# Performance work log

Measured on AMD Instinct MI355X. Metric: run time of the kernel, lower is better.

Reference implementation:

```python
import jax, jax.numpy as jnp
import numpy as np

NEG_INF = -1e30


def setup_inputs() -> dict:
    key = jax.random.key(0)
    k1, k2, k3, k4 = jax.random.split(key, 4)
    B, T, C, H = 4, 4096, 1024, 64
    x = jax.random.normal(k1, (B, T, C), dtype=jnp.float32)
    Wk = jax.random.normal(k2, (C, H), dtype=jnp.float32) * (C ** -0.5)
    Wq = jax.random.normal(k3, (C, H), dtype=jnp.float32) * (C ** -0.5)
    Wv = jax.random.normal(k4, (C, H), dtype=jnp.float32) * (C ** -0.5)
    return {"x": x, "Wk": Wk, "Wq": Wq, "Wv": Wv}


def reference(x, Wk, Wq, Wv):
    # x: [B, T, C]; Wq/Wk/Wv: [C, H]
    B, T, C = x.shape
    q = jnp.einsum('btc,ch->bth', x, Wq)  # [B,T,H]
    k = jnp.einsum('btc,ch->bth', x, Wk)  # [B,T,H]
    v = jnp.einsum('btc,ch->bth', x, Wv)  # [B,T,H]
    # NOTE: original scales by C**-0.5 (n_embd), not head_size**-0.5.
    scale = jnp.asarray(C, x.dtype) ** -0.5
    wei = jnp.einsum('bth,bsh->bts', q, k) * scale  # [B,T,T]
    causal = jnp.tril(jnp.ones((T, T), dtype=bool))
    wei = jnp.where(causal, wei, NEG_INF)
    wei = jax.nn.softmax(wei, axis=-1)
    # dropout p=0.0 -> identity
    out = jnp.einsum('bts,bsh->bth', wei, v)  # [B,T,H]
    return out
```

## Files before the change

kernel.cpp:

```cpp
#include <hip/hip_runtime.h>
#include <math.h>

typedef short bfx8 __attribute__((ext_vector_type(8)));
typedef short bfx4 __attribute__((ext_vector_type(4)));
typedef float fx4  __attribute__((ext_vector_type(4)));

__device__ __forceinline__ unsigned short f2bf(float f) {
    unsigned int u = __builtin_bit_cast(unsigned int, f);
    u += 0x7FFFu + ((u >> 16) & 1u);
    return (unsigned short)(u >> 16);
}
__device__ __forceinline__ float bf2f(unsigned short s) {
    unsigned int u = ((unsigned int)s) << 16;
    return __builtin_bit_cast(float, u);
}

__global__ __launch_bounds__(256) void wt_prep(const float* __restrict__ Wq,
                                               const float* __restrict__ Wk,
                                               const float* __restrict__ Wv,
                                               unsigned short* __restrict__ wt)
{
    const int k0  = blockIdx.x * 64;
    const int mat = blockIdx.y;
    const float* W = (mat == 0) ? Wq : ((mat == 1) ? Wk : Wv);
    const float scale = (mat == 0) ? (0.03125f * 1.4426950408889634f) : 1.0f;
    __shared__ unsigned short Ls[64 * 68];
    const int t = threadIdx.x;
    #pragma unroll
    for (int i = 0; i < 4; ++i) {
        int idx4 = t + 256 * i;
        int r = idx4 >> 4, c4 = idx4 & 15;
        float4 v = *(const float4*)&W[(size_t)(k0 + r) * 64 + c4 * 4];
        Ls[r * 68 + c4 * 4 + 0] = f2bf(v.x * scale);
        Ls[r * 68 + c4 * 4 + 1] = f2bf(v.y * scale);
        Ls[r * 68 + c4 * 4 + 2] = f2bf(v.z * scale);
        Ls[r * 68 + c4 * 4 + 3] = f2bf(v.w * scale);
    }
    __syncthreads();
    #pragma unroll
    for (int i = 0; i < 2; ++i) {
        int u = t + 256 * i;
        int n = u >> 3, kc = u & 7;
        bfx8 o;
        #pragma unroll
        for (int j = 0; j < 8; ++j) o[j] = (short)Ls[(kc * 8 + j) * 68 + n];
        *(bfx8*)&wt[(size_t)(mat * 64 + n) * 1024 + k0 + kc * 8] = o;
    }
}

__global__ __launch_bounds__(256) void qkv_mfma(
    const float* __restrict__ x, const unsigned short* __restrict__ wt,
    unsigned short* __restrict__ qb, unsigned short* __restrict__ kb,
    unsigned short* __restrict__ vt)
{
    __shared__ alignas(16) char smem[57344];
    const int t = threadIdx.x;
    const int w = t >> 6, l = t & 63, g = l >> 4, li = l & 15;
    const int m0 = blockIdx.x * 32;
    const int rh  = (w & 1) * 16;
    const int nb0 = (w >> 1) * 6;

    fx4 acc[6];
    #pragma unroll
    for (int i = 0; i < 6; ++i) acc[i] = (fx4){0.f, 0.f, 0.f, 0.f};

    float4 xr[2]; bfx8 wr[6];

#define QKV_LOAD(K0) do { \
    _Pragma("unroll") for (int i_ = 0; i_ < 2; ++i_) { int idx4 = t + 256 * i_; int r_ = idx4 >> 4, c4 = idx4 & 15; \
        xr[i_] = *(const float4*)&x[(size_t)(m0 + r_) * 1024 + (K0) + c4 * 4]; } \
    _Pragma("unroll") for (int i_ = 0; i_ < 6; ++i_) { int idx = t + 256 * i_; int n_ = idx >> 3, c_ = idx & 7; \
        wr[i_] = *(const bfx8*)&wt[(size_t)n_ * 1024 + (K0) + c_ * 8]; } \
} while (0)

#define QKV_STORE(BI) do { \
    char* xb_ = smem + (BI) * 4096; \
    char* wb_ = smem + 8192 + (BI) * 24576; \
    _Pragma("unroll") for (int i_ = 0; i_ < 2; ++i_) { int idx4 = t + 256 * i_; int r_ = idx4 >> 4, c4 = idx4 & 15; \
        bfx4 o_; o_[0] = (short)f2bf(xr[i_].x); o_[1] = (short)f2bf(xr[i_].y); \
        o_[2] = (short)f2bf(xr[i_].z); o_[3] = (short)f2bf(xr[i_].w); \
        *(bfx4*)(xb_ + ((r_ * 128 + c4 * 8) ^ ((r_ & 7) << 4))) = o_; } \
    _Pragma("unroll") for (int i_ = 0; i_ < 6; ++i_) { int idx = t + 256 * i_; int n_ = idx >> 3, c_ = idx & 7; \
        *(bfx8*)(wb_ + ((n_ * 128 + c_ * 16) ^ ((n_ & 7) << 4))) = wr[i_]; } \
} while (0)

    QKV_LOAD(0); QKV_STORE(0);
    __syncthreads();

    for (int ch = 0; ch < 16; ++ch) {
        if (ch + 1 < 16) QKV_LOAD((ch + 1) * 64);
        if (ch) __syncthreads();
        char* xb = smem + (ch & 1) * 4096;
        char* wb = smem + 8192 + (ch & 1) * 24576;
        const int arow = rh + li;
        #pragma unroll
        for (int kk = 0; kk < 2; ++kk) {
            bfx8 af = *(bfx8*)(xb + ((arow * 128 + kk * 64 + g * 16) ^ ((arow & 7) << 4)));
            #pragma unroll
            for (int nb = 0; nb < 6; ++nb) {
                int nrow = (nb0 + nb) * 16 + li;
                bfx8 bf = *(bfx8*)(wb + ((nrow * 128 + kk * 64 + g * 16) ^ ((nrow & 7) << 4)));
                acc[nb] = __builtin_amdgcn_mfma_f32_16x16x32_bf16(af, bf, acc[nb], 0, 0, 0);
            }
        }
        if (ch + 1 < 16) QKV_STORE((ch + 1) & 1);
    }

    const int mrow = m0 + rh + g * 4;
    #pragma unroll
    for (int nb = 0; nb < 6; ++nb) {
        const int nbg = nb0 + nb;
        if (nbg < 4) {
            #pragma unroll
            for (int r = 0; r < 4; ++r)
                qb[(size_t)(mrow + r) * 64 + nbg * 16 + li] = f2bf(acc[nb][r]);
        } else if (nbg < 8) {
            #pragma unroll
            for (int r = 0; r < 4; ++r)
                kb[(size_t)(mrow + r) * 64 + (nbg - 4) * 16 + li] = f2bf(acc[nb][r]);
        }
    }

    __syncthreads();
    unsigned short* Vt = (unsigned short*)smem;
    #pragma unroll
    for (int nb = 0; nb < 6; ++nb) {
        const int nbg = nb0 + nb;
        if (nbg >= 8) {
            #pragma unroll
            for (int r = 0; r < 4; ++r)
                Vt[((nbg - 8) * 16 + li) * 40 + g * 8 + (rh >> 2) + r] = f2bf(acc[nb][r]);
        }
    }
    __syncthreads();
    const int bb = m0 >> 12, mt = m0 & 4095;
    {
        int d = t >> 2, c = t & 3;
        *(bfx8*)&vt[((size_t)(bb * 64 + d)) * 4096 + mt + c * 8] = *(bfx8*)&Vt[d * 40 + c * 8];
    }
}

__global__ __launch_bounds__(256, 4) void attn_mfma(
    const unsigned short* __restrict__ qb, const unsigned short* __restrict__ kb,
    const unsigned short* __restrict__ vt,
    unsigned short* __restrict__ pO, float* __restrict__ pml)
{
    __shared__ alignas(16) char smem[34816];
    const int t = threadIdx.x;
    const int w = t >> 6, l = t & 63, g = l >> 4, li = l & 15;
    const int bx = blockIdx.x;

    const int b = bx & 3;
    const int j = bx >> 2;
    int qt, seg, nch;
    if (j < 224) {
        int a = 1;
        #pragma unroll
        for (int aa = 2; aa <= 7; ++aa) if (j >= 4 * aa * (aa - 1)) a = aa;
        const int local = j - 4 * a * (a - 1);
        qt = 8 * a + local / a;
        seg = local % a;
        nch = 8;
    } else {
        const int jd = j - 224;
        const int r = 7 - (jd >> 3);
        const int a = jd & 7;
        qt = 8 * a + r; seg = a; nch = r + 1;
    }
    const int qbase = qt * 64;
    const int kvb = seg * 512;
    const int qsub = w & 1, par = w >> 1;
    const int qmax_w = qbase + qsub * 32 + 31;
    const int aq = qt >> 3, rq = qt & 7;
    const int slot = b * 288 + (aq + 1) * (4 * aq + rq) + seg;

    const unsigned short* Qg = qb + (size_t)b * 4096 * 64;
    const unsigned short* Kg = kb + (size_t)b * 4096 * 64;
    const unsigned short* Vg = vt + (size_t)b * 64 * 4096;

    bfx8 krg[2], vrg[2];

#define ATT_LOAD(CB) do { \
    _Pragma("unroll") for (int i_ = 0; i_ < 2; ++i_) { int idx = t + 256 * i_; int r_ = idx >> 3, c_ = idx & 7; \
        krg[i_] = *(const bfx8*)&Kg[(size_t)((CB) + r_) * 64 + c_ * 8]; } \
    _Pragma("unroll") for (int i_ = 0; i_ < 2; ++i_) { int idx = t + 256 * i_; int d_ = idx >> 3, c_ = idx & 7; \
        vrg[i_] = *(const bfx8*)&Vg[(size_t)d_ * 4096 + (CB) + c_ * 8]; } \
} while (0)

#define ATT_STORE(BI) do { \
    char* kb_ = smem + (BI) * 8192; \
    char* vb_ = smem + 16384 + (BI) * 8192; \
    _Pragma("unroll") for (int i_ = 0; i_ < 2; ++i_) { int idx = t + 256 * i_; int r_ = idx >> 3, c_ = idx & 7; \
        *(bfx8*)(kb_ + ((r_ * 128 + c_ * 16) ^ ((r_ & 7) << 4))) = krg[i_]; } \
    _Pragma("unroll") for (int i_ = 0; i_ < 2; ++i_) { int idx = t + 256 * i_; int d_ = idx >> 3, c_ = idx & 7; \
        *(bfx8*)(vb_ + ((d_ * 128 + c_ * 16) ^ ((d_ & 7) << 4))) = vrg[i_]; } \
} while (0)

    bfx8 qf[2][2];
    #pragma unroll
    for (int f = 0; f < 2; ++f)
        #pragma unroll
        for (int h = 0; h < 2; ++h)
            qf[f][h] = *(const bfx8*)&Qg[(size_t)(qbase + qsub * 32 + f * 16 + li) * 64 + h * 32 + g * 8];

    ATT_LOAD(kvb); ATT_STORE(0);
    __syncthreads();

    fx4 o[4][2];
    #pragma unroll
    for (int i = 0; i < 4; ++i)
        #pragma unroll
        for (int f = 0; f < 2; ++f) o[i][f] = (fx4){0.f, 0.f, 0.f, 0.f};
    float lsum[2] = {0.f, 0.f};

    for (int ch = 0; ch < nch; ++ch) {
        const int cb = kvb + (ch << 6);
        if (ch + 1 < nch) ATT_LOAD(cb + 64);
        char* ks = smem + (ch & 1) * 8192;
        char* vs = smem + 16384 + (ch & 1) * 8192;
        const int sub = cb + par * 32;
        if (sub <= qmax_w) {
            fx4 s[2][2];
            #pragma unroll
            for (int st = 0; st < 2; ++st)
                #pragma unroll
                for (int f = 0; f < 2; ++f) s[st][f] = (fx4){0.f, 0.f, 0.f, 0.f};
            __builtin_amdgcn_s_setprio(1);
            #pragma unroll
            for (int st = 0; st < 2; ++st) {
                const int krow = par * 32 + st * 16 + li;
                const int sw = (krow & 7) << 4;
                bfx8 kf0 = *(bfx8*)(ks + ((krow * 128 + g * 16) ^ sw));
                bfx8 kf1 = *(bfx8*)(ks + ((krow * 128 + 64 + g * 16) ^ sw));
                #pragma unroll
                for (int f = 0; f < 2; ++f) {
                    s[st][f] = __builtin_amdgcn_mfma_f32_16x16x32_bf16(kf0, qf[f][0], s[st][f], 0, 0, 0);
                    s[st][f] = __builtin_amdgcn_mfma_f32_16x16x32_bf16(kf1, qf[f][1], s[st][f], 0, 0, 0);
                }
            }
            __builtin_amdgcn_s_setprio(0);

            bfx8 pf[2];
            #pragma unroll
            for (int f = 0; f < 2; ++f) {
                const int qmin_f = qbase + qsub * 32 + f * 16;
                float p[8];
                if (sub + 31 > qmin_f) {
                    #pragma unroll
                    for (int st = 0; st < 2; ++st)
                        #pragma unroll
                        for (int rr = 0; rr < 4; ++rr) {
                            int kv = sub + st * 16 + 4 * g + rr;
                            p[st * 4 + rr] = (kv <= qmin_f + li) ? s[st][f][rr] : -1e30f;
                        }
                } else {
                    #pragma unroll
                    for (int st = 0; st < 2; ++st)
                        #pragma unroll
                        for (int rr = 0; rr < 4; ++rr) p[st * 4 + rr] = s[st][f][rr];
                }
                #pragma unroll
                for (int e = 0; e < 8; ++e) p[e] = exp2f(p[e]);
                lsum[f] += ((p[0]+p[1])+(p[2]+p[3])) + ((p[4]+p[5])+(p[6]+p[7]));
                #pragma unroll
                for (int e = 0; e < 8; ++e) pf[f][e] = (short)f2bf(p[e]);
            }

            __builtin_amdgcn_s_setprio(1);
            #pragma unroll
            for (int dblk = 0; dblk < 4; ++dblk) {
                const int dr = dblk * 16 + li;
                bfx8 vf = *(bfx8*)(vs + ((dr * 128 + par * 64 + g * 16) ^ ((dr & 7) << 4)));
                #pragma unroll
                for (int f = 0; f < 2; ++f)
                    o[dblk][f] = __builtin_amdgcn_mfma_f32_16x16x32_bf16(vf, pf[f], o[dblk][f], 0, 0, 0);
            }
            __builtin_amdgcn_s_setprio(0);
        }
        if (ch + 1 < nch) ATT_STORE((ch + 1) & 1);
        __syncthreads();
    }

    float* Osh = (float*)smem;
    float* lsh = (float*)(smem + 32768);
    #pragma unroll
    for (int dblk = 0; dblk < 4; ++dblk)
        #pragma unroll
        for (int f = 0; f < 2; ++f)
            #pragma unroll
            for (int r = 0; r < 4; ++r)
                Osh[(par * 64 + qsub * 32 + f * 16 + li) * 64 + dblk * 16 + g * 4 + r] = o[dblk][f][r];
    #pragma unroll
    for (int f = 0; f < 2; ++f)
        lsh[((w * 2 + f) * 4 + g) * 16 + li] = lsum[f];
    __syncthreads();

    {
        const int q = t >> 2, dg = t & 3;
        const int A = (q >> 5), Bw = A + 2, fq = (q >> 4) & 1, liq = q & 15;
        float L = 0.f;
        #pragma unroll
        for (int gg2 = 0; gg2 < 4; ++gg2)
            L += lsh[((A * 2 + fq) * 4 + gg2) * 16 + liq] + lsh[((Bw * 2 + fq) * 4 + gg2) * 16 + liq];
        const float* OA = &Osh[q * 64 + dg * 16];
        const float* OB = &Osh[(64 + q) * 64 + dg * 16];
        bfx8 o1_, o2_;
        #pragma unroll
        for (int jj = 0; jj < 8; ++jj) o1_[jj] = (short)f2bf(OA[jj] + OB[jj]);
        #pragma unroll
        for (int jj = 0; jj < 8; ++jj) o2_[jj] = (short)f2bf(OA[8 + jj] + OB[8 + jj]);
        unsigned short* dst = pO + (size_t)slot * 4096 + q * 64 + dg * 16;
        *(bfx8*)&dst[0] = o1_;
        *(bfx8*)&dst[8] = o2_;
        if (dg == 0) pml[(size_t)slot * 64 + q] = L;
    }
}

__global__ __launch_bounds__(256) void attn_merge(
    const unsigned short* __restrict__ pO, const float* __restrict__ pml,
    float* __restrict__ out)
{
    const int b = blockIdx.x & 3, qt = blockIdx.x >> 2;
    const int a = qt >> 3, r = qt & 7;
    const int nseg = a + 1;
    const int slot0 = b * 288 + (a + 1) * (4 * a + r);
    const int t = threadIdx.x;
    const int q = t >> 2, dg = t & 3;

    float L = 0.f;
    float acc[16];
    #pragma unroll
    for (int jj = 0; jj < 16; ++jj) acc[jj] = 0.f;
    #pragma unroll
    for (int s = 0; s < 8; ++s) {
        if (s < nseg) {
            L += pml[(size_t)(slot0 + s) * 64 + q];
            const unsigned short* src = pO + (size_t)(slot0 + s) * 4096 + q * 64 + dg * 16;
            bfx8 v0 = *(const bfx8*)&src[0];
            bfx8 v1 = *(const bfx8*)&src[8];
            #pragma unroll
            for (int jj = 0; jj < 8; ++jj) acc[jj]     += bf2f((unsigned short)v0[jj]);
            #pragma unroll
            for (int jj = 0; jj < 8; ++jj) acc[8 + jj] += bf2f((unsigned short)v1[jj]);
        }
    }
    const float inv = 1.f / L;
    float* orow = out + ((size_t)b * 4096 + qt * 64 + q) * 64 + dg * 16;
    #pragma unroll
    for (int v4 = 0; v4 < 4; ++v4) {
        float4 rr;
        rr.x = acc[v4 * 4 + 0] * inv; rr.y = acc[v4 * 4 + 1] * inv;
        rr.z = acc[v4 * 4 + 2] * inv; rr.w = acc[v4 * 4 + 3] * inv;
        *(float4*)&orow[v4 * 4] = rr;
    }
}

extern "C" void kernel_launch(void* const* d_in, const int* in_sizes, int n_in,
                              void* d_out, int out_size, void* d_ws, size_t ws_size,
                              hipStream_t stream)
{
    const float* x  = (const float*)d_in[0];
    const float* Wk = (const float*)d_in[1];
    const float* Wq = (const float*)d_in[2];
    const float* Wv = (const float*)d_in[3];
    float* outp = (float*)d_out;

    char* ws = (char*)d_ws;
    unsigned short* qbuf = (unsigned short*)(ws);
    unsigned short* kbuf = (unsigned short*)(ws + 2*1024*1024);
    unsigned short* vtb  = (unsigned short*)(ws + 4*1024*1024);
    unsigned short* wtb  = (unsigned short*)(ws + 6*1024*1024);
    unsigned short* pO   = (unsigned short*)(ws + 7*1024*1024);
    float*          pml  = (float*)(ws + 16*1024*1024 + 512*1024);

    wt_prep<<<dim3(16, 3), 256, 0, stream>>>(Wq, Wk, Wv, wtb);
    qkv_mfma<<<512, 256, 0, stream>>>(x, wtb, qbuf, kbuf, vtb);
    attn_mfma<<<1152, 256, 0, stream>>>(qbuf, kbuf, vtb, pO, pml);
    attn_merge<<<256, 256, 0, stream>>>(pO, pml, outp);
}
```

Before: 57.33 us.

## Use direct global-to-LDS loads for W/K/V tiles and packed bf16 conversions

Replaces the register-staged loads and swizzled LDS stores of the weight tiles (QKV projection) and the K/V tiles (attention) with global_load_lds DMA. The XOR swizzle is folded into per-lane source addresses so the LDS layout stays the same. It also replaces scalar bf16 rounding with the hardware v_cvt_pk_bf16_f32 packed conversion in the x staging, P fragments and output epilogue. The aim is to free VGPRs and VALU issue slots spent on staging and conversion. The risk is in the async-load synchronization, since there is no explicit vmcnt wait before the barrier, and conversion rounding may differ slightly.

Result: no change. 56.55 us (-1.4%).

```diff
diff --git a/kernel.cpp b/kernel.cpp
--- a/kernel.cpp
+++ b/kernel.cpp
@@ -4,6 +4,8 @@
 typedef short bfx8 __attribute__((ext_vector_type(8)));
 typedef short bfx4 __attribute__((ext_vector_type(4)));
 typedef float fx4  __attribute__((ext_vector_type(4)));
+typedef unsigned int ux2 __attribute__((ext_vector_type(2)));
+typedef unsigned int ux4v __attribute__((ext_vector_type(4)));
 
 __device__ __forceinline__ unsigned short f2bf(float f) {
     unsigned int u = __builtin_bit_cast(unsigned int, f);
@@ -13,6 +15,11 @@
 __device__ __forceinline__ float bf2f(unsigned short s) {
     unsigned int u = ((unsigned int)s) << 16;
     return __builtin_bit_cast(float, u);
+}
+__device__ __forceinline__ unsigned int cvtpk(float a, float b) {
+    unsigned int d;
+    asm("v_cvt_pk_bf16_f32 %0, %1, %2" : "=v"(d) : "v"(a), "v"(b));
+    return d;
 }
 
 __global__ __launch_bounds__(256) void wt_prep(const float* __restrict__ Wq,
@@ -64,32 +71,41 @@
     #pragma unroll
     for (int i = 0; i < 6; ++i) acc[i] = (fx4){0.f, 0.f, 0.f, 0.f};
 
-    float4 xr[2]; bfx8 wr[6];
-
-#define QKV_LOAD(K0) do { \
+    float4 xr[2];
+
+    const unsigned short* wSrc[6];
+    #pragma unroll
+    for (int i = 0; i < 6; ++i) {
+        int s = w * 6144 + i * 1024 + l * 16;
+        int n = s >> 7, c = ((s >> 4) & 7) ^ (n & 7);
+        wSrc[i] = wt + (size_t)n * 1024 + c * 8;
+    }
+
+#define QKV_DMA_W(K0, BI) do { \
+    _Pragma("unroll") for (int i_ = 0; i_ < 6; ++i_) \
+        __builtin_amdgcn_global_load_lds( \
+            (const __attribute__((address_space(1))) void*)(wSrc[i_] + (K0)), \
+            (__attribute__((address_space(3))) void*)(smem + 8192 + (BI) * 24576 + w * 6144 + i_ * 1024), \
+            16, 0, 0); \
+} while (0)
+
+#define QKV_LOAD_X(K0) do { \
     _Pragma("unroll") for (int i_ = 0; i_ < 2; ++i_) { int idx4 = t + 256 * i_; int r_ = idx4 >> 4, c4 = idx4 & 15; \
         xr[i_] = *(const float4*)&x[(size_t)(m0 + r_) * 1024 + (K0) + c4 * 4]; } \
-    _Pragma("unroll") for (int i_ = 0; i_ < 6; ++i_) { int idx = t + 256 * i_; int n_ = idx >> 3, c_ = idx & 7; \
-        wr[i_] = *(const bfx8*)&wt[(size_t)n_ * 1024 + (K0) + c_ * 8]; } \
 } while (0)
 
-#define QKV_STORE(BI) do { \
+#define QKV_STORE_X(BI) do { \
     char* xb_ = smem + (BI) * 4096; \
-    char* wb_ = smem + 8192 + (BI) * 24576; \
     _Pragma("unroll") for (int i_ = 0; i_ < 2; ++i_) { int idx4 = t + 256 * i_; int r_ = idx4 >> 4, c4 = idx4 & 15; \
-        bfx4 o_; o_[0] = (short)f2bf(xr[i_].x); o_[1] = (short)f2bf(xr[i_].y); \
-        o_[2] = (short)f2bf(xr[i_].z); o_[3] = (short)f2bf(xr[i_].w); \
-        *(bfx4*)(xb_ + ((r_ * 128 + c4 * 8) ^ ((r_ & 7) << 4))) = o_; } \
-    _Pragma("unroll") for (int i_ = 0; i_ < 6; ++i_) { int idx = t + 256 * i_; int n_ = idx >> 3, c_ = idx & 7; \
-        *(bfx8*)(wb_ + ((n_ * 128 + c_ * 16) ^ ((n_ & 7) << 4))) = wr[i_]; } \
+        ux2 u_; u_[0] = cvtpk(xr[i_].x, xr[i_].y); u_[1] = cvtpk(xr[i_].z, xr[i_].w); \
+        *(ux2*)(xb_ + ((r_ * 128 + c4 * 8) ^ ((r_ & 7) << 4))) = u_; } \
 } while (0)
 
-    QKV_LOAD(0); QKV_STORE(0);
+    QKV_LOAD_X(0); QKV_STORE_X(0); QKV_DMA_W(0, 0);
     __syncthreads();
 
     for (int ch = 0; ch < 16; ++ch) {
-        if (ch + 1 < 16) QKV_LOAD((ch + 1) * 64);
-        if (ch) __syncthreads();
+        if (ch + 1 < 16) { QKV_DMA_W((ch + 1) * 64, (ch + 1) & 1); QKV_LOAD_X((ch + 1) * 64); }
         char* xb = smem + (ch & 1) * 4096;
         char* wb = smem + 8192 + (ch & 1) * 24576;
         const int arow = rh + li;
@@ -103,7 +119,8 @@
                 acc[nb] = __builtin_amdgcn_mfma_f32_16x16x32_bf16(af, bf, acc[nb], 0, 0, 0);
             }
         }
-        if (ch + 1 < 16) QKV_STORE((ch + 1) & 1);
+        if (ch + 1 < 16) QKV_STORE_X((ch + 1) & 1);
+        __syncthreads();
     }
 
     const int mrow = m0 + rh + g * 4;
@@ -178,22 +195,24 @@
     const unsigned short* Kg = kb + (size_t)b * 4096 * 64;
     const unsigned short* Vg = vt + (size_t)b * 64 * 4096;
 
-    bfx8 krg[2], vrg[2];
-
-#define ATT_LOAD(CB) do { \
-    _Pragma("unroll") for (int i_ = 0; i_ < 2; ++i_) { int idx = t + 256 * i_; int r_ = idx >> 3, c_ = idx & 7; \
-        krg[i_] = *(const bfx8*)&Kg[(size_t)((CB) + r_) * 64 + c_ * 8]; } \
-    _Pragma("unroll") for (int i_ = 0; i_ < 2; ++i_) { int idx = t + 256 * i_; int d_ = idx >> 3, c_ = idx & 7; \
-        vrg[i_] = *(const bfx8*)&Vg[(size_t)d_ * 4096 + (CB) + c_ * 8]; } \
-} while (0)
-
-#define ATT_STORE(BI) do { \
-    char* kb_ = smem + (BI) * 8192; \
-    char* vb_ = smem + 16384 + (BI) * 8192; \
-    _Pragma("unroll") for (int i_ = 0; i_ < 2; ++i_) { int idx = t + 256 * i_; int r_ = idx >> 3, c_ = idx & 7; \
-        *(bfx8*)(kb_ + ((r_ * 128 + c_ * 16) ^ ((r_ & 7) << 4))) = krg[i_]; } \
-    _Pragma("unroll") for (int i_ = 0; i_ < 2; ++i_) { int idx = t + 256 * i_; int d_ = idx >> 3, c_ = idx & 7; \
-        *(bfx8*)(vb_ + ((d_ * 128 + c_ * 16) ^ ((d_ & 7) << 4))) = vrg[i_]; } \
+    const unsigned short* kSrc[2];
+    const unsigned short* vSrc[2];
+    #pragma unroll
+    for (int i = 0; i < 2; ++i) {
+        int s = w * 2048 + i * 1024 + l * 16;
+        int r = s >> 7, c = ((s >> 4) & 7) ^ (r & 7);
+        kSrc[i] = Kg + (size_t)r * 64 + c * 8;
+        vSrc[i] = Vg + (size_t)r * 4096 + c * 8;
+    }
+
+#define ATT_DMA(CB, BI) do { \
+    _Pragma("unroll") for (int i_ = 0; i_ < 2; ++i_) { \
+        __builtin_amdgcn_global_load_lds( \
+            (const __attribute__((address_space(1))) void*)(kSrc[i_] + (size_t)(CB) * 64), \
+            (__attribute__((address_space(3))) void*)(smem + (BI) * 8192 + w * 2048 + i_ * 1024), 16, 0, 0); \
+        __builtin_amdgcn_global_load_lds( \
+            (const __attribute__((address_space(1))) void*)(vSrc[i_] + (CB)), \
+            (__attribute__((address_space(3))) void*)(smem + 16384 + (BI) * 8192 + w * 2048 + i_ * 1024), 16, 0, 0); } \
 } while (0)
 
     bfx8 qf[2][2];
@@ -203,7 +222,7 @@
         for (int h = 0; h < 2; ++h)
             qf[f][h] = *(const bfx8*)&Qg[(size_t)(qbase + qsub * 32 + f * 16 + li) * 64 + h * 32 + g * 8];
 
-    ATT_LOAD(kvb); ATT_STORE(0);
+    ATT_DMA(kvb, 0);
     __syncthreads();
 
     fx4 o[4][2];
@@ -215,7 +234,7 @@
 
     for (int ch = 0; ch < nch; ++ch) {
         const int cb = kvb + (ch << 6);
-        if (ch + 1 < nch) ATT_LOAD(cb + 64);
+        if (ch + 1 < nch) ATT_DMA(cb + 64, (ch + 1) & 1);
         char* ks = smem + (ch & 1) * 8192;
         char* vs = smem + 16384 + (ch & 1) * 8192;
         const int sub = cb + par * 32;
@@ -262,8 +281,10 @@
                 #pragma unroll
                 for (int e = 0; e < 8; ++e) p[e] = exp2f(p[e]);
                 lsum[f] += ((p[0]+p[1])+(p[2]+p[3])) + ((p[4]+p[5])+(p[6]+p[7]));
-                #pragma unroll
-                for (int e = 0; e < 8; ++e) pf[f][e] = (short)f2bf(p[e]);
+                ux4v pu;
+                pu[0] = cvtpk(p[0], p[1]); pu[1] = cvtpk(p[2], p[3]);
+                pu[2] = cvtpk(p[4], p[5]); pu[3] = cvtpk(p[6], p[7]);
+                pf[f] = __builtin_bit_cast(bfx8, pu);
             }
 
             __builtin_amdgcn_s_setprio(1);
@@ -277,7 +298,6 @@
             }
             __builtin_amdgcn_s_setprio(0);
         }
-        if (ch + 1 < nch) ATT_STORE((ch + 1) & 1);
         __syncthreads();
     }
 
@@ -304,14 +324,18 @@
             L += lsh[((A * 2 + fq) * 4 + gg2) * 16 + liq] + lsh[((Bw * 2 + fq) * 4 + gg2) * 16 + liq];
         const float* OA = &Osh[q * 64 + dg * 16];
         const float* OB = &Osh[(64 + q) * 64 + dg * 16];
-        bfx8 o1_, o2_;
-        #pragma unroll
-        for (int jj = 0; jj < 8; ++jj) o1_[jj] = (short)f2bf(OA[jj] + OB[jj]);
-        #pragma unroll
-        for (int jj = 0; jj < 8; ++jj) o2_[jj] = (short)f2bf(OA[8 + jj] + OB[8 + jj]);
+        ux4v u1, u2;
+        u1[0] = cvtpk(OA[0] + OB[0],  OA[1] + OB[1]);
+        u1[1] = cvtpk(OA[2] + OB[2],  OA[3] + OB[3]);
+        u1[2] = cvtpk(OA[4] + OB[4],  OA[5] + OB[5]);
+        u1[3] = cvtpk(OA[6] + OB[6],  OA[7] + OB[7]);
+        u2[0] = cvtpk(OA[8] + OB[8],  OA[9] + OB[9]);
+        u2[1] = cvtpk(OA[10] + OB[10], OA[11] + OB[11]);
+        u2[2] = cvtpk(OA[12] + OB[12], OA[13] + OB[13]);
+        u2[3] = cvtpk(OA[14] + OB[14], OA[15] + OB[15]);
         unsigned short* dst = pO + (size_t)slot * 4096 + q * 64 + dg * 16;
-        *(bfx8*)&dst[0] = o1_;
-        *(bfx8*)&dst[8] = o2_;
+        *(bfx8*)&dst[0] = __builtin_bit_cast(bfx8, u1);
+        *(bfx8*)&dst[8] = __builtin_bit_cast(bfx8, u2);
         if (dg == 0) pml[(size_t)slot * 64 + q] = L;
     }
 }
```
